# Kernel tuning notes

Measured on AMD Instinct MI355X. Metric: run time of the kernel, lower is better.

## Reference

```python
import jax, jax.numpy as jnp
import numpy as np

B, L, V, E = 8, 2000, 50000, 300      # batch, doc len, vocab, embed dim
NL, LW = 8922, 10                     # num labels, words per label desc
F_, K, H = 200, 10, 200               # num_filters, kernel_size, label_hidden
FEAT = E + H                          # feat_size = 500


def setup_inputs():
    key = jax.random.key(0)
    ks = jax.random.split(key, 12)
    n = lambda k, sh, s=0.02: jax.random.normal(k, sh, jnp.float32) * s
    x = jax.random.randint(ks[0], (B, L), 0, V)
    y = (jax.random.uniform(ks[1], (B, NL)) < 0.01).astype(jnp.float32)
    mask = jnp.ones((B, L), jnp.float32)
    word_emb = n(ks[2], (V, E), 0.1)
    label_idx_matrix = jax.random.randint(ks[3], (NL, LW), 0, V)
    label_idx_mask = jnp.ones((NL, LW), jnp.float32)
    adj_matrix = (jax.random.uniform(ks[4], (NL, NL)) < 0.002).astype(jnp.float32)
    num_neighbors = jnp.maximum(adj_matrix.sum(axis=1), 1.0)
    return {
        'x': x, 'y': y, 'mask': mask,
        'word_emb': word_emb,
        'label_idx_matrix': label_idx_matrix,
        'label_idx_mask': label_idx_mask,
        'adj_matrix': adj_matrix,
        'num_neighbors': num_neighbors,
        'Wg': n(ks[5], (E, H)), 'bg': jnp.zeros((H,), jnp.float32),
        'Wc': n(ks[6], (F_, E, K)), 'bc': jnp.zeros((F_,), jnp.float32),
        'Wp': n(ks[7], (F_, E)), 'bp': jnp.zeros((E,), jnp.float32),
        'Wo': n(ks[8], (F_, FEAT)), 'bo': jnp.zeros((FEAT,), jnp.float32),
    }


def reference(x, y, mask, word_emb, label_idx_matrix, label_idx_mask,
              adj_matrix, num_neighbors, Wg, bg, Wc, bc, Wp, bp, Wo, bo):
    # --- average label embedding over label description words ---
    le = word_emb[label_idx_matrix]                              # [NL, LW, E]
    avg = (le * label_idx_mask[..., None]).sum(1)
    avg = avg / label_idx_mask.sum(axis=-1, keepdims=True)       # [NL, E]
    # --- conv graph encoder over label hierarchy ---
    agg = (adj_matrix @ avg) / num_neighbors[:, None]            # [NL, E]
    gh = jax.nn.relu(agg @ Wg + bg)                              # [NL, H]
    graph_emb = jnp.concatenate([avg, gh], axis=-1)              # [NL, FEAT]
    # --- document encoding (dropouts are identity in eval) ---
    xe = word_emb[x] * mask[..., None]                           # [B, L, E]
    c = jax.lax.conv_general_dilated(
        xe.transpose(0, 2, 1), Wc, window_strides=(1,), padding='VALID',
        dimension_numbers=('NCH', 'OIH', 'NCH')) + bc[None, :, None]
    c = jax.nn.relu(c).transpose(0, 2, 1)                        # [B, Lp, F]
    pj = jnp.tanh(c @ Wp + bp)                                   # [B, Lp, E]
    # --- label-wise attention ---
    scores = jnp.einsum('ble,ne->bnl', pj, avg)                  # [B, NL, Lp]
    attn = jax.nn.softmax(scores, axis=-1)
    attn_out = jnp.einsum('bnl,blf->bnf', attn, c)               # [B, NL, F]
    proj = jax.nn.relu(attn_out @ Wo + bo)                       # [B, NL, FEAT]
    logits = (graph_emb[None] * proj).sum(-1)                    # [B, NL]
    # --- BCE-with-logits (sum) / batch ---
    bce = jnp.maximum(logits, 0.0) - logits * y + jnp.log1p(jnp.exp(-jnp.abs(logits)))
    loss = bce.sum() / B
    return (logits, loss)
```

## Files before the change

kernel.cpp:

```cpp
#include <hip/hip_runtime.h>
#include <math.h>

#define B_    8
#define L_    2000
#define V_    50000
#define E_    300
#define NL_   8922
#define NLP_  8960
#define LW_   10
#define F_    200
#define KW_   10
#define H_    200
#define FEAT_ 500
#define LP_   1991

typedef __attribute__((ext_vector_type(8))) short bf16x8;
typedef __attribute__((ext_vector_type(4))) float f32x4;

static __device__ __forceinline__ unsigned short f2b(float f) {
  unsigned u = __builtin_bit_cast(unsigned, f);
  u += 0x7FFF + ((u >> 16) & 1);
  return (unsigned short)(u >> 16);
}
static __device__ __forceinline__ unsigned short f2b_t(float f) {
  return (unsigned short)(__builtin_bit_cast(unsigned, f) >> 16);
}
static __device__ __forceinline__ float b2f(unsigned short u) {
  unsigned v = ((unsigned)u) << 16;
  return __builtin_bit_cast(float, v);
}
static __device__ __forceinline__ float fast_tanh(float x) {
  x = fminf(fmaxf(x, -10.f), 10.f);
  float t = __expf(2.f * x);
  return (t - 1.f) / (t + 1.f);
}
static __device__ __forceinline__ void stage16(const void* g, void* l) {
  __builtin_amdgcn_global_load_lds(
      (const __attribute__((address_space(1))) unsigned int*)g,
      (__attribute__((address_space(3))) unsigned int*)l, 16, 0, 0);
}

#define MFMA(a, b, c) __builtin_amdgcn_mfma_f32_16x16x32_bf16(a, b, c, 0, 0, 0)


__global__ __launch_bounds__(256) void k_avg(const float* __restrict__ we,
                                             const int* __restrict__ lidx,
                                             const float* __restrict__ lmask,
                                             float* __restrict__ avg,
                                             unsigned short* __restrict__ avgb,
                                             unsigned short* __restrict__ geF) {
  int idx = blockIdx.x * 256 + threadIdx.x;
  if (idx >= NLP_ * 80) return;
  int n = idx / 80, e4 = idx - n * 80;
  if (n >= NL_ || e4 >= 75) {
    *(ushort4*)&avgb[(size_t)n * 320 + e4 * 4] = make_ushort4(0, 0, 0, 0);
    return;
  }
  float ax = 0.f, ay = 0.f, az = 0.f, aw = 0.f, ms = 0.f;
#pragma unroll
  for (int w = 0; w < LW_; ++w) {
    float mw = lmask[n * LW_ + w];
    const float4 f = *(const float4*)&we[(size_t)lidx[n * LW_ + w] * E_ + e4 * 4];
    ax = fmaf(f.x, mw, ax); ay = fmaf(f.y, mw, ay);
    az = fmaf(f.z, mw, az); aw = fmaf(f.w, mw, aw);
    ms += mw;
  }
  float inv = 1.f / ms;
  float4 v = {ax * inv, ay * inv, az * inv, aw * inv};
  *(float4*)&avg[(size_t)n * 300 + e4 * 4] = v;
  *(ushort4*)&avgb[(size_t)n * 320 + e4 * 4] =
      make_ushort4(f2b(v.x), f2b(v.y), f2b(v.z), f2b(v.w));
  int ntg = n >> 4, quad = (n >> 2) & 3, r = n & 3;
  int ftg = (e4 * 4) >> 4, c0 = (e4 * 4) & 15;
  size_t tb = (((size_t)ntg * 32 + ftg) << 8);
  float vv[4] = {v.x, v.y, v.z, v.w};
#pragma unroll
  for (int t = 0; t < 4; ++t)
    geF[(tb + quad * 16 + c0 + t) * 4 + r] = f2b(vv[t]);
}

__global__ __launch_bounds__(256) void k_agg(const float* __restrict__ adj,
                                             const float* __restrict__ avg,
                                             const float* __restrict__ nnb,
                                             unsigned short* __restrict__ aggF) {
  __shared__ int s_idx[1024];
  __shared__ float s_val[1024];
  __shared__ float s_agg[320];
  __shared__ int s_cnt;
  const int n = blockIdx.x;
  const int tid = threadIdx.x;
  if (tid == 0) s_cnt = 0;
  __syncthreads();
  const float2* row2 = (const float2*)(adj + (size_t)n * NL_);
  for (int j = tid; j < NL_ / 2; j += 256) {
    float2 v = row2[j];
    if (v.x != 0.f) {
      int p = atomicAdd(&s_cnt, 1);
      if (p < 1024) { s_idx[p] = 2 * j; s_val[p] = v.x; }
    }
    if (v.y != 0.f) {
      int p = atomicAdd(&s_cnt, 1);
      if (p < 1024) { s_idx[p] = 2 * j + 1; s_val[p] = v.y; }
    }
  }
  __syncthreads();
  const int m = min(s_cnt, 1024);
  const float inv = 1.f / nnb[n];
  float a0 = 0.f, a1 = 0.f;
  for (int i = 0; i < m; ++i) {
    const float* ar = avg + (size_t)s_idx[i] * 300;
    float v = s_val[i];
    a0 = fmaf(v, ar[tid], a0);
    if (tid < E_ - 256) a1 = fmaf(v, ar[tid + 256], a1);
  }
  s_agg[tid] = a0 * inv;
  if (tid < E_ - 256) s_agg[tid + 256] = a1 * inv;
  if (tid >= 44 && tid < 64) s_agg[tid + 256] = 0.f;
  __syncthreads();
  if (tid < 320) {
    int e = tid;
    int ks = e >> 5, qA = (e >> 3) & 3, jj = e & 7;
    aggF[(((size_t)((n >> 4) * 10 + ks)) << 9) + ((qA << 4) + (n & 15)) * 8 + jj] =
        f2b(s_agg[e]);
  }
}

__global__ __launch_bounds__(256) void k_gh2(const unsigned short* __restrict__ aggF,
                                             const unsigned short* __restrict__ WgF,
                                             const float* __restrict__ bg,
                                             unsigned short* __restrict__ geF) {
  const int n0g = blockIdx.x * 64;
  const int tid = threadIdx.x;
  const int wv = tid >> 6, lane = tid & 63, quad = lane >> 4, c16 = lane & 15;
  const int mt = wv;
  f32x4 acc[14];
#pragma unroll
  for (int nt = 0; nt < 14; ++nt) acc[nt] = (f32x4){0.f, 0.f, 0.f, 0.f};
#pragma unroll
  for (int ks = 0; ks < 10; ++ks) {
    bf16x8 a = *(const bf16x8*)
        &aggF[(((size_t)(((n0g >> 4) + mt) * 10 + ks)) << 9) + (lane << 3)];
#pragma unroll
    for (int nt = 0; nt < 14; ++nt) {
      bf16x8 bw = *(const bf16x8*)&WgF[(((size_t)(nt * 10 + ks)) << 9) + (lane << 3)];
      acc[nt] = MFMA(a, bw, acc[nt]);
    }
  }
#pragma unroll
  for (int nt = 0; nt < 14; ++nt) {
    int h = nt * 16 + c16;
    if (h < H_) {
      float bgv = bg[h];
      int feat = 300 + h;
      int ftg = feat >> 4, cg = feat & 15;
#pragma unroll
      for (int r = 0; r < 4; ++r) {
        int n = n0g + mt * 16 + quad * 4 + r;
        if (n < NL_)
          geF[((((size_t)(n >> 4) * 32 + ftg) << 8) + (quad << 4) + cg) * 4 + r] =
              f2b(fmaxf(acc[nt][r] + bgv, 0.f));
      }
    }
  }
}

__global__ __launch_bounds__(256) void k_wprep(const float* __restrict__ Wc,
                                               const float* __restrict__ Wp,
                                               const float* __restrict__ Wo,
                                               const float* __restrict__ Wg,
                                               unsigned short* __restrict__ WcF,
                                               unsigned short* __restrict__ WpF,
                                               unsigned short* __restrict__ WoF,
                                               unsigned short* __restrict__ WgF) {
  int idx = blockIdx.x * 256 + threadIdx.x;
  if (idx < 819200) {
    int koff = idx / (16 * 10 * 512);
    int rem = idx - koff * (16 * 10 * 512);
    int ft = rem / (10 * 512);
    int rem2 = rem - ft * (10 * 512);
    int ks = rem2 >> 9, t = rem2 & 511;
    int lane = t >> 3, j = t & 7;
    int f = ft * 16 + (lane & 15);
    int e = ks * 32 + (lane >> 4) * 8 + j;
    float v = (f < F_ && e < E_) ? Wc[((size_t)f * E_ + e) * KW_ + koff] : 0.f;
    WcF[idx] = f2b(v);
    return;
  }
  idx -= 819200;
  if (idx < 71680) {
    int et = idx / (7 * 512);
    int rem = idx - et * (7 * 512);
    int kt = rem >> 9, t = rem & 511;
    int lane = t >> 3, j = t & 7;
    int e = et * 16 + (lane & 15);
    int f = kt * 32 + (lane >> 4) * 8 + j;
    float v = (e < E_ && f < F_) ? Wp[(size_t)f * E_ + e] : 0.f;
    WpF[idx] = f2b(v);
    return;
  }
  idx -= 71680;
  if (idx < 114688) {
    int g = idx / (7 * 512);
    int rem = idx - g * (7 * 512);
    int kt = rem >> 9, t = rem & 511;
    int lane = t >> 3, j = t & 7;
    int feat = g * 16 + (lane & 15);
    int f = kt * 32 + (lane >> 4) * 8 + j;
    float v = (feat < FEAT_ && f < F_) ? Wo[(size_t)f * FEAT_ + feat] : 0.f;
    WoF[idx] = f2b(v);
    return;
  }
  idx -= 114688;
  if (idx < 71680) {
    int nt = idx / (10 * 512);
    int rem = idx - nt * (10 * 512);
    int ks = rem >> 9, t = rem & 511;
    int lane = t >> 3, j = t & 7;
    int h = nt * 16 + (lane & 15);
    int e = ks * 32 + (lane >> 4) * 8 + j;
    float v = (h < H_ && e < E_) ? Wg[(size_t)e * H_ + h] : 0.f;
    WgF[idx] = f2b(v);
  }
}

__global__ __launch_bounds__(256) void k_cpj(const int* __restrict__ x,
                                             const float* __restrict__ mask,
                                             const float* __restrict__ we,
                                             const unsigned short* __restrict__ WcF,
                                             const float* __restrict__ bc,
                                             const unsigned short* __restrict__ WpF,
                                             const float* __restrict__ bp,
                                             unsigned short* __restrict__ cF,
                                             unsigned short* __restrict__ pjF) {
  __shared__ __attribute__((aligned(16))) unsigned char smem[78896];
  unsigned short* s_xe  = (unsigned short*)smem;
  unsigned short* s_pjF = (unsigned short*)smem;
  unsigned short* s_cA  = (unsigned short*)(smem + 50224);

  const int b = blockIdx.y;
  const int l0 = blockIdx.x * 64;
  const int tid = threadIdx.x;
  const int wv = tid >> 6, lane = tid & 63, quad = lane >> 4, c16 = lane & 15;

  for (int i = tid; i < 73 * 75; i += 256) {
    int row = i / 75, e4 = i - row * 75;
    int l = l0 + row;
    float4 v = {0.f, 0.f, 0.f, 0.f};
    if (l < L_) {
      int bl = b * L_ + l;
      v = *(const float4*)&we[(size_t)x[bl] * E_ + e4 * 4];
      float mm = mask[bl];
      v.x *= mm; v.y *= mm; v.z *= mm; v.w *= mm;
    }
    *(ushort4*)&s_xe[row * 344 + e4 * 4] =
        make_ushort4(f2b(v.x), f2b(v.y), f2b(v.z), f2b(v.w));
  }
  for (int i = tid; i < 73 * 5; i += 256) {
    int row = i / 5, c = i - row * 5;
    *(ushort4*)&s_xe[row * 344 + (75 + c) * 4] = make_ushort4(0, 0, 0, 0);
  }
  __syncthreads();

  f32x4 acc[4][4];
#pragma unroll
  for (int mt = 0; mt < 4; ++mt)
#pragma unroll
    for (int j = 0; j < 4; ++j) acc[mt][j] = (f32x4){0.f, 0.f, 0.f, 0.f};
  for (int koff = 0; koff < KW_; ++koff) {
#pragma unroll
    for (int ks = 0; ks < 10; ++ks) {
      bf16x8 a[4];
#pragma unroll
      for (int mt = 0; mt < 4; ++mt)
        a[mt] = *(const bf16x8*)&s_xe[(mt * 16 + c16 + koff) * 344 + ks * 32 + quad * 8];
#pragma unroll
      for (int jj = 0; jj < 4; ++jj) {
        bf16x8 bw = *(const bf16x8*)
            &WcF[(((size_t)((koff * 16 + wv * 4 + jj) * 10 + ks)) << 9) + (lane << 3)];
#pragma unroll
        for (int mt = 0; mt < 4; ++mt) acc[mt][jj] = MFMA(a[mt], bw, acc[mt][jj]);
      }
    }
  }
  unsigned short* cFb = cF + (size_t)b * (16 * 64 * 512);
#pragma unroll
  for (int jj = 0; jj < 4; ++jj) {
    const int ft2 = wv * 4 + jj;
    const int f = ft2 * 16 + c16;
    const float bcv = (f < F_) ? bc[f] : 0.f;
    const int kt = ft2 >> 1;
    const int qA = ((ft2 & 1) << 1) | (c16 >> 3);
    const int jA = c16 & 7;
#pragma unroll
    for (int mt = 0; mt < 4; ++mt) {
      unsigned short u[4];
#pragma unroll
      for (int r = 0; r < 4; ++r) u[r] = f2b(fmaxf(acc[mt][jj][r] + bcv, 0.f));
      int su = (l0 >> 5) + (mt >> 1);
      int lane_c = ((((mt & 1) << 1) | (quad >> 1)) << 4) + c16;
      *(ushort4*)&cFb[(((size_t)(ft2 * 64 + su)) << 9) + lane_c * 8 + ((quad & 1) << 2)] =
          make_ushort4(u[0], u[1], u[2], u[3]);
      if (ft2 < 14) {
#pragma unroll
        for (int r = 0; r < 4; ++r)
          s_cA[(((size_t)(mt * 7 + kt)) << 9) + ((qA << 4) + quad * 4 + r) * 8 + jA] = u[r];
      }
    }
  }
  __syncthreads();

  f32x4 pacc[4][5];
#pragma unroll
  for (int mt = 0; mt < 4; ++mt)
#pragma unroll
    for (int j = 0; j < 5; ++j) pacc[mt][j] = (f32x4){0.f, 0.f, 0.f, 0.f};
#pragma unroll
  for (int kt = 0; kt < 7; ++kt) {
    bf16x8 a[4];
#pragma unroll
    for (int mt = 0; mt < 4; ++mt)
      a[mt] = *(const bf16x8*)&s_cA[(((size_t)(mt * 7 + kt)) << 9) + (lane << 3)];
#pragma unroll
    for (int j = 0; j < 5; ++j) {
      bf16x8 bw = *(const bf16x8*)
          &WpF[(((size_t)((wv * 5 + j) * 7 + kt)) << 9) + (lane << 3)];
#pragma unroll
      for (int mt = 0; mt < 4; ++mt) pacc[mt][j] = MFMA(a[mt], bw, pacc[mt][j]);
    }
  }
  __syncthreads();
#pragma unroll
  for (int j = 0; j < 5; ++j) {
    const int et = wv * 5 + j;
    const int e = et * 16 + c16;
    const float bpe = (e < E_) ? bp[e] : 0.f;
    const int ks = et >> 1;
    const int qP = ((et & 1) << 1) | (c16 >> 3);
    const int jP = c16 & 7;
#pragma unroll
    for (int mt = 0; mt < 4; ++mt) {
#pragma unroll
      for (int r = 0; r < 4; ++r) {
        float v = (e < E_) ? fast_tanh(pacc[mt][j][r] + bpe) : 0.f;
        s_pjF[(((size_t)(mt * 10 + ks)) << 9) + ((qP << 4) + quad * 4 + r) * 8 + jP] = f2b(v);
      }
    }
  }
  __syncthreads();
  {
    unsigned short* dst = pjF + (((size_t)((b * 128 + (l0 >> 4)) * 10)) << 9);
    for (int i = tid; i < 2560; i += 256)
      *(uint4*)&dst[i * 8] = *(const uint4*)&s_pjF[i * 8];
  }
}

__global__ __launch_bounds__(256, 2) void k_attn(
    const unsigned short* __restrict__ pjF,
    const unsigned short* __restrict__ cF,
    const unsigned short* __restrict__ avgb,
    const unsigned short* __restrict__ WoF,
    const unsigned short* __restrict__ geF,
    const float* __restrict__ bo,
    float* __restrict__ out) {
  __shared__ __attribute__((aligned(16))) unsigned char smem[78848];
  unsigned short* Ps  = (unsigned short*)(smem + 69632);
  float* s_wsum = (float*)(smem + 77824);
  float* s_sum  = (float*)(smem + 78336);
  float* s_lg   = (float*)(smem + 78592);
  unsigned short* AOs = (unsigned short*)smem;

  const int tid = threadIdx.x;
  const int b  = blockIdx.x & 7;
  const int n0 = (blockIdx.x >> 3) << 6;
  const int wv = tid >> 6, lane = tid & 63, quad = lane >> 4, c16 = lane & 15;
  const int lh = wv & 1, nh = wv >> 1;

  if (tid < 64) s_lg[tid] = 0.f;

  bf16x8 bavg[10][2];
#pragma unroll
  for (int ks = 0; ks < 10; ++ks)
#pragma unroll
    for (int nt = 0; nt < 2; ++nt)
      bavg[ks][nt] = *(const bf16x8*)
          &avgb[(size_t)(n0 + nh * 32 + nt * 16 + c16) * 320 + ks * 32 + quad * 8];

  const unsigned short* pjb = pjF + (size_t)b * (128 * 10 * 512);
  const unsigned short* cFb = cF + (size_t)b * (16 * 64 * 512);

  {
    const unsigned char* pg = (const unsigned char*)pjb;
#pragma unroll
    for (int t = 0; t < 5; ++t) {
      int off = (wv * 5 + t) << 10;
      stage16(pg + off + lane * 16, smem + off);
    }
  }

  f32x4 o[2][7];
#pragma unroll
  for (int nt = 0; nt < 2; ++nt)
#pragma unroll
    for (int j = 0; j < 7; ++j) o[nt][j] = (f32x4){0.f, 0.f, 0.f, 0.f};
  float ssum[2] = {0.f, 0.f};

  for (int c = 0; c < 64; ++c) {
    __builtin_amdgcn_s_waitcnt(0);
    __syncthreads();
    const int cb = c & 1;
    const unsigned short* pjcur = (const unsigned short*)(smem + cb * 20480);
    const unsigned short* cfprev = (const unsigned short*)(smem + 40960 + (cb ^ 1) * 14336);
    if (c + 1 < 64) {
      const unsigned char* pg =
          (const unsigned char*)pjb + (((size_t)((c + 1) * 20)) << 10);
#pragma unroll
      for (int t = 0; t < 5; ++t) {
        int off = (wv * 5 + t) << 10;
        stage16(pg + off + lane * 16, smem + (cb ^ 1) * 20480 + off);
      }
    }
#pragma unroll
    for (int t = 0; t < 4; ++t) {
      int ft = wv + t * 4;
      if (ft < 14)
        stage16((const unsigned char*)cFb + (((size_t)(ft * 64 + c)) << 10) + lane * 16,
                smem + 40960 + cb * 14336 + (ft << 10));
    }
    f32x4 acc0 = (f32x4){0.f, 0.f, 0.f, 0.f};
    f32x4 acc1 = (f32x4){0.f, 0.f, 0.f, 0.f};
#pragma unroll
    for (int ks = 0; ks < 10; ++ks) {
      bf16x8 a = *(const bf16x8*)(pjcur + ((lh * 10 + ks) << 9) + (lane << 3));
      acc0 = MFMA(a, bavg[ks][0], acc0);
      acc1 = MFMA(a, bavg[ks][1], acc1);
    }
    if (c) {
      const unsigned short* Pp = Ps + ((cb ^ 1) << 11);
      bf16x8 aP0 = *(const bf16x8*)(Pp + ((nh * 2) << 9) + (lane << 3));
      bf16x8 aP1 = *(const bf16x8*)(Pp + ((nh * 2 + 1) << 9) + (lane << 3));
#pragma unroll
      for (int ft = 0; ft < 7; ++ft) {
        bf16x8 bC = *(const bf16x8*)(cfprev + ((lh * 7 + ft) << 9) + (lane << 3));
        o[0][ft] = MFMA(aP0, bC, o[0][ft]);
        o[1][ft] = MFMA(aP1, bC, o[1][ft]);
      }
    }
    {
      unsigned short* Pc = Ps + (cb << 11);
      const int lb = (c << 5) + lh * 16 + quad * 4;
#pragma unroll
      for (int nt = 0; nt < 2; ++nt) {
        f32x4 av = nt ? acc1 : acc0;
        float psum = 0.f;
        unsigned short u[4];
#pragma unroll
        for (int r = 0; r < 4; ++r) {
          float p = __expf(av[r]);
          if (c >= 62 && (lb + r >= LP_)) p = 0.f;
          u[r] = f2b_t(p);
          psum += b2f(u[r]);
        }
        *(ushort4*)&Pc[((nh * 2 + nt) << 9) +
                       ((lh * 2 + (quad >> 1)) * 16 + c16) * 8 + ((quad & 1) << 2)] =
            make_ushort4(u[0], u[1], u[2], u[3]);
        psum += __shfl_xor(psum, 16);
        psum += __shfl_xor(psum, 32);
        ssum[nt] += psum;
      }
    }
  }
  __builtin_amdgcn_s_waitcnt(0);
  __syncthreads();
  {
    const unsigned short* cfprev = (const unsigned short*)(smem + 40960 + 14336);
    const unsigned short* Pp = Ps + (1 << 11);
    bf16x8 aP0 = *(const bf16x8*)(Pp + ((nh * 2) << 9) + (lane << 3));
    bf16x8 aP1 = *(const bf16x8*)(Pp + ((nh * 2 + 1) << 9) + (lane << 3));
#pragma unroll
    for (int ft = 0; ft < 7; ++ft) {
      bf16x8 bC = *(const bf16x8*)(cfprev + ((lh * 7 + ft) << 9) + (lane << 3));
      o[0][ft] = MFMA(aP0, bC, o[0][ft]);
      o[1][ft] = MFMA(aP1, bC, o[1][ft]);
    }
  }

  if (lane < 16) {
    s_wsum[wv * 32 + lane] = ssum[0];
    s_wsum[wv * 32 + 16 + lane] = ssum[1];
  }
  __syncthreads();
  if (tid < 64) {
    int g = tid >> 5, idx = tid & 31;
    s_sum[tid] = s_wsum[(g * 2) * 32 + idx] + s_wsum[(g * 2 + 1) * 32 + idx];
  }
  __syncthreads();
#pragma unroll
  for (int nt = 0; nt < 2; ++nt) {
    const int ntile = nh * 2 + nt;
    float inv4[4];
#pragma unroll
    for (int r = 0; r < 4; ++r) inv4[r] = 1.f / s_sum[ntile * 16 + quad * 4 + r];
#pragma unroll
    for (int ft = 0; ft < 7; ++ft) {
      int f = (lh * 7 + ft) * 16 + c16;
      int kt = f >> 5, qA = (f >> 3) & 3, jA = f & 7;
#pragma unroll
      for (int r = 0; r < 4; ++r)
        AOs[((ntile * 7 + kt) << 9) + ((qA << 4) + quad * 4 + r) * 8 + jA] =
            f2b(o[nt][ft][r] * inv4[r]);
    }
  }
  __syncthreads();
  float la[4][4];
#pragma unroll
  for (int nt = 0; nt < 4; ++nt)
#pragma unroll
    for (int r = 0; r < 4; ++r) la[nt][r] = 0.f;
#pragma unroll
  for (int i = 0; i < 8; ++i) {
    const int ftg = wv * 8 + i;
    const int feat = (ftg << 4) + c16;
    f32x4 pa[4];
#pragma unroll
    for (int nt = 0; nt < 4; ++nt) pa[nt] = (f32x4){0.f, 0.f, 0.f, 0.f};
    const unsigned short* wof = WoF + (((size_t)(ftg * 7)) << 9) + (lane << 3);
#pragma unroll
    for (int kt = 0; kt < 7; ++kt) {
      bf16x8 bw = *(const bf16x8*)(wof + (kt << 9));
#pragma unroll
      for (int nt = 0; nt < 4; ++nt) {
        bf16x8 aa = *(const bf16x8*)&AOs[((nt * 7 + kt) << 9) + (lane << 3)];
        pa[nt] = MFMA(aa, bw, pa[nt]);
      }
    }
    const float bof = (feat < FEAT_) ? bo[feat] : 0.f;
#pragma unroll
    for (int nt = 0; nt < 4; ++nt) {
      ushort4 g4 = *(const ushort4*)
          &geF[((((size_t)(n0 >> 4) + nt) * 32 + ftg) << 8) + (lane << 2)];
      float gv[4] = {b2f(g4.x), b2f(g4.y), b2f(g4.z), b2f(g4.w)};
#pragma unroll
      for (int r = 0; r < 4; ++r) {
        float pv = fmaxf(pa[nt][r] + bof, 0.f);
        la[nt][r] = fmaf(pv, gv[r], la[nt][r]);
      }
    }
  }
#pragma unroll
  for (int nt = 0; nt < 4; ++nt)
#pragma unroll
    for (int r = 0; r < 4; ++r) {
      float v = la[nt][r];
      v += __shfl_xor(v, 1); v += __shfl_xor(v, 2);
      v += __shfl_xor(v, 4); v += __shfl_xor(v, 8);
      if (c16 == 0) atomicAdd(&s_lg[nt * 16 + quad * 4 + r], v);
    }
  __syncthreads();
  if (tid < 64) {
    int ng = n0 + tid;
    if (ng < NL_) out[(size_t)b * NL_ + ng] = s_lg[tid];
  }
}

__global__ __launch_bounds__(1024) void k_loss(const float* __restrict__ lgts,
                                               const float* __restrict__ y,
                                               float* __restrict__ loss) {
  __shared__ float red[1024];
  const int tid = threadIdx.x;
  float s = 0.f;
  for (int i = tid; i < B_ * NL_; i += 1024) {
    float l = lgts[i], yy = y[i];
    s += fmaxf(l, 0.f) - l * yy + log1pf(expf(-fabsf(l)));
  }
  red[tid] = s;
  __syncthreads();
  for (int st = 512; st > 0; st >>= 1) {
    if (tid < st) red[tid] += red[tid + st];
    __syncthreads();
  }
  if (tid == 0) loss[0] = red[0] * (1.f / B_);
}

extern "C" void kernel_launch(void* const* d_in, const int* in_sizes, int n_in,
                              void* d_out, int out_size, void* d_ws, size_t ws_size,
                              hipStream_t stream) {
  const int*   x     = (const int*)  d_in[0];
  const float* y     = (const float*)d_in[1];
  const float* mask  = (const float*)d_in[2];
  const float* we    = (const float*)d_in[3];
  const int*   lidx  = (const int*)  d_in[4];
  const float* lmask = (const float*)d_in[5];
  const float* adj   = (const float*)d_in[6];
  const float* nnb   = (const float*)d_in[7];
  const float* Wg    = (const float*)d_in[8];
  const float* bg    = (const float*)d_in[9];
  const float* Wc    = (const float*)d_in[10];
  const float* bc    = (const float*)d_in[11];
  const float* Wp    = (const float*)d_in[12];
  const float* bp    = (const float*)d_in[13];
  const float* Wo    = (const float*)d_in[14];
  const float* bo    = (const float*)d_in[15];
  float* out = (float*)d_out;
  char* W = (char*)d_ws;

  unsigned short* pjF  = (unsigned short*)(W + 0);
  unsigned short* cF   = (unsigned short*)(W + 10485760);
  unsigned short* avgb = (unsigned short*)(W + 18874368);
  unsigned short* geF  = (unsigned short*)(W + 24608768);
  unsigned short* aggF = (unsigned short*)(W + 33783808);
  unsigned short* WcF  = (unsigned short*)(W + 44490208);
  unsigned short* WpF  = (unsigned short*)(W + 46128608);
  unsigned short* WoF  = (unsigned short*)(W + 46271968);
  unsigned short* WgF  = (unsigned short*)(W + 46501344);
  float*          avg  = (float*)(W + 0);

  hipMemsetAsync(geF, 0, 9175040, stream);
  k_wprep<<<(819200 + 71680 + 114688 + 71680 + 255) / 256, 256, 0, stream>>>(
      Wc, Wp, Wo, Wg, WcF, WpF, WoF, WgF);
  k_avg<<<(NLP_ * 80 + 255) / 256, 256, 0, stream>>>(we, lidx, lmask, avg, avgb, geF);
  k_agg<<<NL_, 256, 0, stream>>>(adj, avg, nnb, aggF);
  k_gh2<<<140, 256, 0, stream>>>(aggF, WgF, bg, geF);
  k_cpj<<<dim3(32, B_), 256, 0, stream>>>(x, mask, we, WcF, bc, WpF, bp, cF, pjF);
  k_attn<<<140 * 8, 256, 0, stream>>>(pjF, cF, avgb, WoF, geF, bo, out);
  k_loss<<<1, 1024, 0, stream>>>(out, y, out + B_ * NL_);
}
```

Baseline: 992.6 us.

## Single-buffer attention kernel and remap waves to label tiles for occupancy

```diff
diff --git a/kernel.cpp b/kernel.cpp
--- a/kernel.cpp
+++ b/kernel.cpp
@@ -354,7 +354,7 @@
   }
 }
 
-__global__ __launch_bounds__(256, 2) void k_attn(
+__global__ __launch_bounds__(256, 3) void k_attn(
     const unsigned short* __restrict__ pjF,
     const unsigned short* __restrict__ cF,
     const unsigned short* __restrict__ avgb,
@@ -362,31 +362,27 @@
     const unsigned short* __restrict__ geF,
     const float* __restrict__ bo,
     float* __restrict__ out) {
-  __shared__ __attribute__((aligned(16))) unsigned char smem[78848];
-  unsigned short* Ps  = (unsigned short*)(smem + 69632);
-  float* s_wsum = (float*)(smem + 77824);
-  float* s_sum  = (float*)(smem + 78336);
-  float* s_lg   = (float*)(smem + 78592);
+  __shared__ __attribute__((aligned(16))) unsigned char smem[39424];
+  float* s_sum = (float*)(smem + 38912);
+  float* s_lg  = (float*)(smem + 39168);
   unsigned short* AOs = (unsigned short*)smem;
 
   const int tid = threadIdx.x;
   const int b  = blockIdx.x & 7;
   const int n0 = (blockIdx.x >> 3) << 6;
   const int wv = tid >> 6, lane = tid & 63, quad = lane >> 4, c16 = lane & 15;
-  const int lh = wv & 1, nh = wv >> 1;
 
   if (tid < 64) s_lg[tid] = 0.f;
 
-  bf16x8 bavg[10][2];
+  bf16x8 bavg[10];
 #pragma unroll
   for (int ks = 0; ks < 10; ++ks)
-#pragma unroll
-    for (int nt = 0; nt < 2; ++nt)
-      bavg[ks][nt] = *(const bf16x8*)
-          &avgb[(size_t)(n0 + nh * 32 + nt * 16 + c16) * 320 + ks * 32 + quad * 8];
+    bavg[ks] = *(const bf16x8*)
+        &avgb[(size_t)(n0 + wv * 16 + c16) * 320 + ks * 32 + quad * 8];
 
   const unsigned short* pjb = pjF + (size_t)b * (128 * 10 * 512);
   const unsigned short* cFb = cF + (size_t)b * (16 * 64 * 512);
+  unsigned short* Pw = (unsigned short*)(smem + 34816 + (wv << 10));
 
   {
     const unsigned char* pg = (const unsigned char*)pjb;
@@ -395,119 +391,101 @@
       int off = (wv * 5 + t) << 10;
       stage16(pg + off + lane * 16, smem + off);
     }
-  }
-
-  f32x4 o[2][7];
-#pragma unroll
-  for (int nt = 0; nt < 2; ++nt)
-#pragma unroll
-    for (int j = 0; j < 7; ++j) o[nt][j] = (f32x4){0.f, 0.f, 0.f, 0.f};
-  float ssum[2] = {0.f, 0.f};
+#pragma unroll
+    for (int t = 0; t < 4; ++t) {
+      int ft = wv + t * 4;
+      if (ft < 14)
+        stage16((const unsigned char*)cFb + (((size_t)(ft * 64)) << 10) + lane * 16,
+                smem + 20480 + (ft << 10));
+    }
+  }
+
+  f32x4 o[14];
+#pragma unroll
+  for (int i = 0; i < 14; ++i) o[i] = (f32x4){0.f, 0.f, 0.f, 0.f};
+  float ssum = 0.f;
 
   for (int c = 0; c < 64; ++c) {
     __builtin_amdgcn_s_waitcnt(0);
     __syncthreads();
-    const int cb = c & 1;
-    const unsigned short* pjcur = (const unsigned short*)(smem + cb * 20480);
-    const unsigned short* cfprev = (const unsigned short*)(smem + 40960 + (cb ^ 1) * 14336);
+    const unsigned short* pt = (const unsigned short*)smem;
+    f32x4 acc0 = (f32x4){0.f, 0.f, 0.f, 0.f};
+    f32x4 acc1 = (f32x4){0.f, 0.f, 0.f, 0.f};
+#pragma unroll
+    for (int ks = 0; ks < 10; ++ks) {
+      bf16x8 a0 = *(const bf16x8*)(pt + (ks << 9) + (lane << 3));
+      bf16x8 a1 = *(const bf16x8*)(pt + ((10 + ks) << 9) + (lane << 3));
+      acc0 = MFMA(a0, bavg[ks], acc0);
+      acc1 = MFMA(a1, bavg[ks], acc1);
+    }
+    {
+      const int lb0 = (c << 5) + quad * 4;
+      float psum = 0.f;
+      unsigned short u[4];
+#pragma unroll
+      for (int r = 0; r < 4; ++r) {
+        float p = __expf(acc0[r]);
+        if (c >= 62 && (lb0 + r >= LP_)) p = 0.f;
+        u[r] = f2b_t(p);
+        psum += b2f(u[r]);
+      }
+      *(ushort4*)&Pw[(((quad >> 1) << 4) + c16) * 8 + ((quad & 1) << 2)] =
+          make_ushort4(u[0], u[1], u[2], u[3]);
+#pragma unroll
+      for (int r = 0; r < 4; ++r) {
+        float p = __expf(acc1[r]);
+        if (c >= 62 && (lb0 + 16 + r >= LP_)) p = 0.f;
+        u[r] = f2b_t(p);
+        psum += b2f(u[r]);
+      }
+      *(ushort4*)&Pw[(((2 + (quad >> 1)) << 4) + c16) * 8 + ((quad & 1) << 2)] =
+          make_ushort4(u[0], u[1], u[2], u[3]);
+      psum += __shfl_xor(psum, 16);
+      psum += __shfl_xor(psum, 32);
+      ssum += psum;
+    }
+    {
+      bf16x8 aP = *(const bf16x8*)&Pw[lane << 3];
+      const unsigned short* cc = (const unsigned short*)(smem + 20480);
+#pragma unroll
+      for (int ft = 0; ft < 14; ++ft) {
+        bf16x8 bC = *(const bf16x8*)(cc + (ft << 9) + (lane << 3));
+        o[ft] = MFMA(aP, bC, o[ft]);
+      }
+    }
+    __syncthreads();
     if (c + 1 < 64) {
       const unsigned char* pg =
           (const unsigned char*)pjb + (((size_t)((c + 1) * 20)) << 10);
 #pragma unroll
       for (int t = 0; t < 5; ++t) {
         int off = (wv * 5 + t) << 10;
-        stage16(pg + off + lane * 16, smem + (cb ^ 1) * 20480 + off);
-      }
-    }
-#pragma unroll
-    for (int t = 0; t < 4; ++t) {
-      int ft = wv + t * 4;
-      if (ft < 14)
-        stage16((const unsigned char*)cFb + (((size_t)(ft * 64 + c)) << 10) + lane * 16,
-                smem + 40960 + cb * 14336 + (ft << 10));
-    }
-    f32x4 acc0 = (f32x4){0.f, 0.f, 0.f, 0.f};
-    f32x4 acc1 = (f32x4){0.f, 0.f, 0.f, 0.f};
-#pragma unroll
-    for (int ks = 0; ks < 10; ++ks) {
-      bf16x8 a = *(const bf16x8*)(pjcur + ((lh * 10 + ks) << 9) + (lane << 3));
-      acc0 = MFMA(a, bavg[ks][0], acc0);
-      acc1 = MFMA(a, bavg[ks][1], acc1);
-    }
-    if (c) {
-      const unsigned short* Pp = Ps + ((cb ^ 1) << 11);
-      bf16x8 aP0 = *(const bf16x8*)(Pp + ((nh * 2) << 9) + (lane << 3));
-      bf16x8 aP1 = *(const bf16x8*)(Pp + ((nh * 2 + 1) << 9) + (lane << 3));
-#pragma unroll
-      for (int ft = 0; ft < 7; ++ft) {
-        bf16x8 bC = *(const bf16x8*)(cfprev + ((lh * 7 + ft) << 9) + (lane << 3));
-        o[0][ft] = MFMA(aP0, bC, o[0][ft]);
-        o[1][ft] = MFMA(aP1, bC, o[1][ft]);
-      }
-    }
-    {
-      unsigned short* Pc = Ps + (cb << 11);
-      const int lb = (c << 5) + lh * 16 + quad * 4;
-#pragma unroll
-      for (int nt = 0; nt < 2; ++nt) {
-        f32x4 av = nt ? acc1 : acc0;
-        float psum = 0.f;
-        unsigned short u[4];
-#pragma unroll
-        for (int r = 0; r < 4; ++r) {
-          float p = __expf(av[r]);
-          if (c >= 62 && (lb + r >= LP_)) p = 0.f;
-          u[r] = f2b_t(p);
-          psum += b2f(u[r]);
-        }
-        *(ushort4*)&Pc[((nh * 2 + nt) << 9) +
-                       ((lh * 2 + (quad >> 1)) * 16 + c16) * 8 + ((quad & 1) << 2)] =
-            make_ushort4(u[0], u[1], u[2], u[3]);
-        psum += __shfl_xor(psum, 16);
-        psum += __shfl_xor(psum, 32);
-        ssum[nt] += psum;
-      }
-    }
-  }
-  __builtin_amdgcn_s_waitcnt(0);
+        stage16(pg + off + lane * 16, smem + off);
+      }
+#pragma unroll
+      for (int t = 0; t < 4; ++t) {
+        int ft = wv + t * 4;
+        if (ft < 14)
+          stage16((const unsigned char*)cFb + (((size_t)(ft * 64 + c + 1)) << 10) + lane * 16,
+                  smem + 20480 + (ft << 10));
+      }
+    }
+  }
+
+  if (lane < 16) s_sum[wv * 16 + lane] = ssum;
   __syncthreads();
   {
-    const unsigned short* cfprev = (const unsigned short*)(smem + 40960 + 14336);
-    const unsigned short* Pp = Ps + (1 << 11);
-    bf16x8 aP0 = *(const bf16x8*)(Pp + ((nh * 2) << 9) + (lane << 3));
-    bf16x8 aP1 = *(const bf16x8*)(Pp + ((nh * 2 + 1) << 9) + (lane << 3));
-#pragma unroll
-    for (int ft = 0; ft < 7; ++ft) {
-      bf16x8 bC = *(const bf16x8*)(cfprev + ((lh * 7 + ft) << 9) + (lane << 3));
-      o[0][ft] = MFMA(aP0, bC, o[0][ft]);
-      o[1][ft] = MFMA(aP1, bC, o[1][ft]);
-    }
-  }
-
-  if (lane < 16) {
-    s_wsum[wv * 32 + lane] = ssum[0];
-    s_wsum[wv * 32 + 16 + lane] = ssum[1];
-  }
-  __syncthreads();
-  if (tid < 64) {
-    int g = tid >> 5, idx = tid & 31;
-    s_sum[tid] = s_wsum[(g * 2) * 32 + idx] + s_wsum[(g * 2 + 1) * 32 + idx];
-  }
-  __syncthreads();
-#pragma unroll
-  for (int nt = 0; nt < 2; ++nt) {
-    const int ntile = nh * 2 + nt;
     float inv4[4];
 #pragma unroll
-    for (int r = 0; r < 4; ++r) inv4[r] = 1.f / s_sum[ntile * 16 + quad * 4 + r];
-#pragma unroll
-    for (int ft = 0; ft < 7; ++ft) {
-      int f = (lh * 7 + ft) * 16 + c16;
+    for (int r = 0; r < 4; ++r) inv4[r] = 1.f / s_sum[wv * 16 + quad * 4 + r];
+#pragma unroll
+    for (int ft = 0; ft < 14; ++ft) {
+      int f = ft * 16 + c16;
       int kt = f >> 5, qA = (f >> 3) & 3, jA = f & 7;
 #pragma unroll
       for (int r = 0; r < 4; ++r)
-        AOs[((ntile * 7 + kt) << 9) + ((qA << 4) + quad * 4 + r) * 8 + jA] =
-            f2b(o[nt][ft][r] * inv4[r]);
+        AOs[((wv * 7 + kt) << 9) + ((qA << 4) + quad * 4 + r) * 8 + jA] =
+            f2b(o[ft][r] * inv4[r]);
     }
   }
   __syncthreads();
```

Result: no change. 1.003 ms (+1.0%).
